# Kernel tuning notes

Hardware: AMD Instinct MI355X
Metric: run time of the kernel (lower is better)

Reference implementation:

```python
import jax, jax.numpy as jnp
import numpy as np

N_NODES = 50000
N_EDGES = 800000
LATDIM = 128
HEAD = 4


def setup_inputs() -> dict:
    key = jax.random.key(0)
    k1, k2, k3, k4, k5, k6 = jax.random.split(key, 6)
    scale = 1.0 / np.sqrt(LATDIM)  # xavier-ish scale for the square projections
    return {
        "embeds": jax.random.normal(k1, (N_NODES, LATDIM), dtype=jnp.float32),
        "qW": jax.random.normal(k2, (LATDIM, LATDIM), dtype=jnp.float32) * scale,
        "kW": jax.random.normal(k3, (LATDIM, LATDIM), dtype=jnp.float32) * scale,
        "vW": jax.random.normal(k4, (LATDIM, LATDIM), dtype=jnp.float32) * scale,
        "rows": jax.random.randint(k5, (N_EDGES,), 0, N_NODES, dtype=jnp.int32),
        "cols": jax.random.randint(k6, (N_EDGES,), 0, N_NODES, dtype=jnp.int32),
    }


def reference(embeds, qW, kW, vW, rows, cols):
    n_nodes, latdim = embeds.shape
    head_dim = latdim // HEAD
    rowEmb = embeds[rows]                         # [E, D] gather by dst
    colEmb = embeds[cols]                         # [E, D] gather by src
    q = (rowEmb @ qW).reshape(-1, HEAD, head_dim)  # [E, H, Dh]
    k = (colEmb @ kW).reshape(-1, HEAD, head_dim)
    v = (colEmb @ vW).reshape(-1, HEAD, head_dim)
    att = jnp.einsum('ehd,ehd->eh', q, k)
    att = jnp.clip(att, -10.0, 10.0)
    expAtt = jnp.exp(att)                          # [E, H]
    # segment softmax denominator via scatter-add over destination nodes
    attNorm = jax.ops.segment_sum(expAtt, rows, num_segments=n_nodes)[rows]
    att = expAtt / (attNorm + 1e-8)
    res = (att[:, :, None] * v).reshape(-1, latdim)  # [E, D]
    out = jax.ops.segment_sum(res, rows, num_segments=n_nodes)  # [N, D]
    return out
```

## Files before the change

kernel.cpp:

```cpp
#include <hip/hip_runtime.h>
#include <hip/hip_bf16.h>

#define N_NODES 50000
#define N_EDGES 800000
#define LATDIM 128
#define HEAD 4
#define SLOT_CAP 96

typedef __attribute__((ext_vector_type(8))) short short8;
typedef __attribute__((ext_vector_type(4))) float floatx4;

__device__ __forceinline__ unsigned bf16_rne_bits(float x) {
    unsigned u = __builtin_bit_cast(unsigned, x);
    return (u + 0x7fffu + ((u >> 16) & 1u)) & 0xffff0000u;
}
__device__ __forceinline__ void split_bf16(float x, short& hi, short& lo) {
    unsigned hb = bf16_rne_bits(x);
    hi = (short)(hb >> 16);
    float hf = __builtin_bit_cast(float, hb);
    unsigned lb = bf16_rne_bits(x - hf);
    lo = (short)(lb >> 16);
}

#define SCAT_T ((N_EDGES / 4 + 767) / 768)
#define GEMM_BLOCKS ((N_NODES + 63) / 64)
#define LDSP 136

__global__ __launch_bounds__(768) void gemm_scatter_kernel(
    const float* __restrict__ E,
    const float* __restrict__ qW, const float* __restrict__ kW,
    const float* __restrict__ vW,
    const int* __restrict__ rows, const int* __restrict__ cols,
    int* __restrict__ cnt, int* __restrict__ slots,
    float* __restrict__ Q, unsigned short* __restrict__ KV2)
{
    __shared__ short AhL[64 * LDSP];
    __shared__ short AlL[64 * LDSP];

    if (blockIdx.x < SCAT_T) {
        const int t = blockIdx.x * 768 + threadIdx.x;
        if (t < N_EDGES / 4) {
            int4 r = ((const int4*)rows)[t];
            int4 c = ((const int4*)cols)[t];
            int p;
            p = atomicAdd(&cnt[r.x], 1);
            if (p < SLOT_CAP) slots[(size_t)r.x * SLOT_CAP + p] = c.x;
            p = atomicAdd(&cnt[r.y], 1);
            if (p < SLOT_CAP) slots[(size_t)r.y * SLOT_CAP + p] = c.y;
            p = atomicAdd(&cnt[r.z], 1);
            if (p < SLOT_CAP) slots[(size_t)r.z * SLOT_CAP + p] = c.z;
            p = atomicAdd(&cnt[r.w], 1);
            if (p < SLOT_CAP) slots[(size_t)r.w * SLOT_CAP + p] = c.w;
        }
        return;
    }

    const int r_base = (blockIdx.x - SCAT_T) * 64;

    for (int chnk = threadIdx.x; chnk < 2048; chnk += 768) {
        const int row = chnk >> 5, c4 = chnk & 31;
        int grow = r_base + row;
        if (grow > N_NODES - 1) grow = N_NODES - 1;
        float4 x = ((const float4*)E)[(size_t)grow * 32 + c4];
        short h0, l0, h1, l1, h2, l2, h3, l3;
        split_bf16(x.x, h0, l0);
        split_bf16(x.y, h1, l1);
        split_bf16(x.z, h2, l2);
        split_bf16(x.w, h3, l3);
        *(short4*)(AhL + row * LDSP + c4 * 4) = make_short4(h0, h1, h2, h3);
        *(short4*)(AlL + row * LDSP + c4 * 4) = make_short4(l0, l1, l2, l3);
    }

    const int wave = threadIdx.x >> 6;
    const int lane = threadIdx.x & 63;
    const int which = wave >> 2;
    const int n_base = (wave & 3) * 32;
    const int ln = lane & 15;
    const int q  = lane >> 4;

    const float* W = (which == 0) ? qW : (which == 1) ? kW : vW;
    short8 Bh[2][4], Bl[2][4];
#pragma unroll
    for (int tIdx = 0; tIdx < 2; ++tIdx)
#pragma unroll
        for (int c = 0; c < 4; ++c)
#pragma unroll
            for (int j = 0; j < 8; ++j) {
                float w = W[(c * 32 + q * 8 + j) * 128 + n_base + tIdx * 16 + ln];
                short hi, lo;
                split_bf16(w, hi, lo);
                Bh[tIdx][c][j] = hi;
                Bl[tIdx][c][j] = lo;
            }

    __syncthreads();

    const int vs = (which == 2) ? 32 : 0;
    const int c0 = n_base + ln;
    const int c1 = n_base + 16 + ln;

    for (int rt = 0; rt < 4; ++rt) {
        const short* ah = AhL + (rt * 16 + ln) * LDSP + q * 8;
        const short* al = AlL + (rt * 16 + ln) * LDSP + q * 8;

        floatx4 acc0 = {0.f, 0.f, 0.f, 0.f};
        floatx4 acc1 = {0.f, 0.f, 0.f, 0.f};
#pragma unroll
        for (int c = 0; c < 4; ++c) {
            short8 Ah = *(const short8*)(ah + c * 32);
            short8 Al = *(const short8*)(al + c * 32);
            acc0 = __builtin_amdgcn_mfma_f32_16x16x32_bf16(Ah, Bh[0][c], acc0, 0, 0, 0);
            acc0 = __builtin_amdgcn_mfma_f32_16x16x32_bf16(Ah, Bl[0][c], acc0, 0, 0, 0);
            acc0 = __builtin_amdgcn_mfma_f32_16x16x32_bf16(Al, Bh[0][c], acc0, 0, 0, 0);
            acc1 = __builtin_amdgcn_mfma_f32_16x16x32_bf16(Ah, Bh[1][c], acc1, 0, 0, 0);
            acc1 = __builtin_amdgcn_mfma_f32_16x16x32_bf16(Ah, Bl[1][c], acc1, 0, 0, 0);
            acc1 = __builtin_amdgcn_mfma_f32_16x16x32_bf16(Al, Bh[1][c], acc1, 0, 0, 0);
        }

        const int r0 = r_base + rt * 16;
#pragma unroll
        for (int r = 0; r < 4; ++r) {
            const int row = r0 + q * 4 + r;
            if (row >= N_NODES) continue;
            if (which == 0) {
                Q[(size_t)row * 128 + c0] = acc0[r];
                Q[(size_t)row * 128 + c1] = acc1[r];
            } else {
                KV2[(size_t)row * 256 + (c0 >> 5) * 64 + (c0 & 31) + vs] =
                    (unsigned short)(bf16_rne_bits(acc0[r]) >> 16);
                KV2[(size_t)row * 256 + (c1 >> 5) * 64 + (c1 & 31) + vs] =
                    (unsigned short)(bf16_rne_bits(acc1[r]) >> 16);
            }
        }
    }
}

__global__ __launch_bounds__(256) void fused_kernel(
    const float* __restrict__ Q,
    const unsigned short* __restrict__ KV2,
    const int* __restrict__ cnt,
    const int* __restrict__ slots,
    float* __restrict__ out)
{
    const int n = blockIdx.x * 4 + (threadIdx.x >> 6);
    if (n >= N_NODES) return;
    const int lane = threadIdx.x & 63;
    const int s  = lane & 1;
    const int h  = (lane >> 1) & 3;
    const int el = lane >> 3;

    int deg = cnt[n];
    if (deg > SLOT_CAP) deg = SLOT_CAP;

    float qv[16];
    {
        const float4* qp = (const float4*)(Q + (size_t)n * 128 + h * 32 + s * 16);
#pragma unroll
        for (int j = 0; j < 4; ++j) {
            float4 t = qp[j];
            qv[4 * j + 0] = t.x; qv[4 * j + 1] = t.y;
            qv[4 * j + 2] = t.z; qv[4 * j + 3] = t.w;
        }
    }

    float acc[16];
#pragma unroll
    for (int j = 0; j < 16; ++j) acc[j] = 0.f;
    float norm = 0.f;

    const int* srow = slots + (size_t)n * SLOT_CAP;

    for (int i = 0; i < deg; i += 8) {
        const int e = i + el;
        if (e < deg) {
            const int col = srow[e];
            const unsigned short* kp = KV2 + (size_t)col * 256 + h * 64 + s * 16;
            uint4 k0 = *(const uint4*)(kp);
            uint4 k1 = *(const uint4*)(kp + 8);
            uint4 v0 = *(const uint4*)(kp + 32);
            uint4 v1 = *(const uint4*)(kp + 40);

            unsigned kw[8] = {k0.x, k0.y, k0.z, k0.w, k1.x, k1.y, k1.z, k1.w};
            float p = 0.f;
#pragma unroll
            for (int d = 0; d < 8; ++d) {
                float flo = __builtin_bit_cast(float, kw[d] << 16);
                float fhi = __builtin_bit_cast(float, kw[d] & 0xffff0000u);
                p += qv[2 * d] * flo + qv[2 * d + 1] * fhi;
            }
            p += __shfl_xor(p, 1);

            float a = expf(fminf(fmaxf(p, -10.0f), 10.0f));
            norm += a;

            unsigned vw[8] = {v0.x, v0.y, v0.z, v0.w, v1.x, v1.y, v1.z, v1.w};
#pragma unroll
            for (int d = 0; d < 8; ++d) {
                float flo = __builtin_bit_cast(float, vw[d] << 16);
                float fhi = __builtin_bit_cast(float, vw[d] & 0xffff0000u);
                acc[2 * d]     += a * flo;
                acc[2 * d + 1] += a * fhi;
            }
        }
    }

#pragma unroll
    for (int m = 8; m <= 32; m <<= 1) {
        norm += __shfl_xor(norm, m, 64);
#pragma unroll
        for (int j = 0; j < 16; ++j) acc[j] += __shfl_xor(acc[j], m, 64);
    }

    if (el == 0) {
        const float inv = 1.0f / (norm + 1e-8f);
        float4* op = (float4*)(out + (size_t)n * 128 + h * 32 + s * 16);
#pragma unroll
        for (int j = 0; j < 4; ++j)
            op[j] = make_float4(acc[4 * j] * inv, acc[4 * j + 1] * inv,
                                acc[4 * j + 2] * inv, acc[4 * j + 3] * inv);
    }
}

extern "C" void kernel_launch(void* const* d_in, const int* in_sizes, int n_in,
                              void* d_out, int out_size, void* d_ws, size_t ws_size,
                              hipStream_t stream) {
    const float* embeds = (const float*)d_in[0];
    const float* qW     = (const float*)d_in[1];
    const float* kW     = (const float*)d_in[2];
    const float* vW     = (const float*)d_in[3];
    const int*   rows   = (const int*)d_in[4];
    const int*   cols   = (const int*)d_in[5];
    float* out = (float*)d_out;

    float* Q = (float*)d_ws;
    unsigned short* KV2 = (unsigned short*)(Q + (size_t)N_NODES * LATDIM);
    int* cnt   = (int*)(KV2 + (size_t)N_NODES * 256);
    int* slots = cnt + N_NODES;

    hipMemsetAsync(cnt, 0, sizeof(int) * N_NODES, stream);

    gemm_scatter_kernel<<<SCAT_T + GEMM_BLOCKS, 768, 0, stream>>>(
        embeds, qW, kW, vW, rows, cols, cnt, slots, Q, KV2);

    fused_kernel<<<(N_NODES + 3) / 4, 256, 0, stream>>>(
        Q, KV2, cnt, slots, out);
}
```

Baseline: 211.9 us.

## Merge scatter, GEMM and attention into one persistent cooperative kernel

```diff
diff --git a/kernel.cpp b/kernel.cpp
--- a/kernel.cpp
+++ b/kernel.cpp
@@ -1,11 +1,21 @@
 #include <hip/hip_runtime.h>
 #include <hip/hip_bf16.h>
+#include <hip/hip_cooperative_groups.h>
+
+namespace cg = cooperative_groups;
 
 #define N_NODES 50000
 #define N_EDGES 800000
 #define LATDIM 128
 #define HEAD 4
 #define SLOT_CAP 96
+
+#define BLOCK_T 768
+#define SCAT_UNITS ((N_EDGES / 4 + BLOCK_T - 1) / BLOCK_T)
+#define GEMM_TILES ((N_NODES + 63) / 64)
+#define FUSE_WAVES 12
+#define FUSE_GROUPS ((N_NODES + FUSE_WAVES - 1) / FUSE_WAVES)
+#define LDSP 136
 
 typedef __attribute__((ext_vector_type(8))) short short8;
 typedef __attribute__((ext_vector_type(4))) float floatx4;
@@ -22,62 +32,55 @@
     lo = (short)(lb >> 16);
 }
 
-#define SCAT_T ((N_EDGES / 4 + 767) / 768)
-#define GEMM_BLOCKS ((N_NODES + 63) / 64)
-#define LDSP 136
-
-__global__ __launch_bounds__(768) void gemm_scatter_kernel(
+__device__ __forceinline__ void scatter_unit(
+    int u, const int* __restrict__ rows, const int* __restrict__ cols,
+    int* __restrict__ cnt, int* __restrict__ slots, int tid)
+{
+    const int t = u * BLOCK_T + tid;
+    if (t < N_EDGES / 4) {
+        int4 r = ((const int4*)rows)[t];
+        int4 c = ((const int4*)cols)[t];
+        int p;
+        p = atomicAdd(&cnt[r.x], 1);
+        if (p < SLOT_CAP) slots[(size_t)r.x * SLOT_CAP + p] = c.x;
+        p = atomicAdd(&cnt[r.y], 1);
+        if (p < SLOT_CAP) slots[(size_t)r.y * SLOT_CAP + p] = c.y;
+        p = atomicAdd(&cnt[r.z], 1);
+        if (p < SLOT_CAP) slots[(size_t)r.z * SLOT_CAP + p] = c.z;
+        p = atomicAdd(&cnt[r.w], 1);
+        if (p < SLOT_CAP) slots[(size_t)r.w * SLOT_CAP + p] = c.w;
+    }
+}
+
+__global__ __launch_bounds__(BLOCK_T) void persist_kernel(
     const float* __restrict__ E,
     const float* __restrict__ qW, const float* __restrict__ kW,
     const float* __restrict__ vW,
     const int* __restrict__ rows, const int* __restrict__ cols,
-    int* __restrict__ cnt, int* __restrict__ slots,
-    float* __restrict__ Q, unsigned short* __restrict__ KV2)
+    int* __restrict__ cnt, int* __restrict__ slots, int* __restrict__ tk,
+    float* __restrict__ Q, unsigned short* __restrict__ KV2,
+    float* __restrict__ out)
 {
     __shared__ short AhL[64 * LDSP];
     __shared__ short AlL[64 * LDSP];
-
-    if (blockIdx.x < SCAT_T) {
-        const int t = blockIdx.x * 768 + threadIdx.x;
-        if (t < N_EDGES / 4) {
-            int4 r = ((const int4*)rows)[t];
-            int4 c = ((const int4*)cols)[t];
-            int p;
-            p = atomicAdd(&cnt[r.x], 1);
-            if (p < SLOT_CAP) slots[(size_t)r.x * SLOT_CAP + p] = c.x;
-            p = atomicAdd(&cnt[r.y], 1);
-            if (p < SLOT_CAP) slots[(size_t)r.y * SLOT_CAP + p] = c.y;
-            p = atomicAdd(&cnt[r.z], 1);
-            if (p < SLOT_CAP) slots[(size_t)r.z * SLOT_CAP + p] = c.z;
-            p = atomicAdd(&cnt[r.w], 1);
-            if (p < SLOT_CAP) slots[(size_t)r.w * SLOT_CAP + p] = c.w;
-        }
-        return;
-    }
-
-    const int r_base = (blockIdx.x - SCAT_T) * 64;
-
-    for (int chnk = threadIdx.x; chnk < 2048; chnk += 768) {
-        const int row = chnk >> 5, c4 = chnk & 31;
-        int grow = r_base + row;
-        if (grow > N_NODES - 1) grow = N_NODES - 1;
-        float4 x = ((const float4*)E)[(size_t)grow * 32 + c4];
-        short h0, l0, h1, l1, h2, l2, h3, l3;
-        split_bf16(x.x, h0, l0);
-        split_bf16(x.y, h1, l1);
-        split_bf16(x.z, h2, l2);
-        split_bf16(x.w, h3, l3);
-        *(short4*)(AhL + row * LDSP + c4 * 4) = make_short4(h0, h1, h2, h3);
-        *(short4*)(AlL + row * LDSP + c4 * 4) = make_short4(l0, l1, l2, l3);
-    }
-
-    const int wave = threadIdx.x >> 6;
-    const int lane = threadIdx.x & 63;
-    const int which = wave >> 2;
+    __shared__ int s_g;
+
+    const int tid  = threadIdx.x;
+    const int wave = tid >> 6;
+    const int lane = tid & 63;
+
+    if (tid == 0) s_g = atomicAdd(&tk[0], 1);
+    __syncthreads();
+    {
+        const int su = s_g;
+        __syncthreads();
+        if (su < SCAT_UNITS) scatter_unit(su, rows, cols, cnt, slots, tid);
+    }
+
+    const int which  = wave >> 2;
     const int n_base = (wave & 3) * 32;
     const int ln = lane & 15;
     const int q  = lane >> 4;
-
     const float* W = (which == 0) ? qW : (which == 1) ? kW : vW;
     short8 Bh[2][4], Bl[2][4];
 #pragma unroll
@@ -93,131 +96,164 @@
                 Bl[tIdx][c][j] = lo;
             }
 
-    __syncthreads();
-
     const int vs = (which == 2) ? 32 : 0;
     const int c0 = n_base + ln;
     const int c1 = n_base + 16 + ln;
 
-    for (int rt = 0; rt < 4; ++rt) {
-        const short* ah = AhL + (rt * 16 + ln) * LDSP + q * 8;
-        const short* al = AlL + (rt * 16 + ln) * LDSP + q * 8;
-
-        floatx4 acc0 = {0.f, 0.f, 0.f, 0.f};
-        floatx4 acc1 = {0.f, 0.f, 0.f, 0.f};
-#pragma unroll
-        for (int c = 0; c < 4; ++c) {
-            short8 Ah = *(const short8*)(ah + c * 32);
-            short8 Al = *(const short8*)(al + c * 32);
-            acc0 = __builtin_amdgcn_mfma_f32_16x16x32_bf16(Ah, Bh[0][c], acc0, 0, 0, 0);
-            acc0 = __builtin_amdgcn_mfma_f32_16x16x32_bf16(Ah, Bl[0][c], acc0, 0, 0, 0);
-            acc0 = __builtin_amdgcn_mfma_f32_16x16x32_bf16(Al, Bh[0][c], acc0, 0, 0, 0);
-            acc1 = __builtin_amdgcn_mfma_f32_16x16x32_bf16(Ah, Bh[1][c], acc1, 0, 0, 0);
-            acc1 = __builtin_amdgcn_mfma_f32_16x16x32_bf16(Ah, Bl[1][c], acc1, 0, 0, 0);
-            acc1 = __builtin_amdgcn_mfma_f32_16x16x32_bf16(Al, Bh[1][c], acc1, 0, 0, 0);
+    for (;;) {
+        if (tid == 0) s_g = atomicAdd(&tk[1], 1);
+        __syncthreads();
+        const int tile = s_g;
+        __syncthreads();
+        if (tile >= GEMM_TILES) break;
+
+        const int r_base = tile * 64;
+        for (int chnk = tid; chnk < 2048; chnk += BLOCK_T) {
+            const int row = chnk >> 5, c4 = chnk & 31;
+            int grow = r_base + row;
+            if (grow > N_NODES - 1) grow = N_NODES - 1;
+            float4 x = ((const float4*)E)[(size_t)grow * 32 + c4];
+            short h0, l0, h1, l1, h2, l2, h3, l3;
+            split_bf16(x.x, h0, l0);
+            split_bf16(x.y, h1, l1);
+            split_bf16(x.z, h2, l2);
+            split_bf16(x.w, h3, l3);
+            *(short4*)(AhL + row * LDSP + c4 * 4) = make_short4(h0, h1, h2, h3);
+            *(short4*)(AlL + row * LDSP + c4 * 4) = make_short4(l0, l1, l2, l3);
         }
-
-        const int r0 = r_base + rt * 16;
-#pragma unroll
-        for (int r = 0; r < 4; ++r) {
-            const int row = r0 + q * 4 + r;
-            if (row >= N_NODES) continue;
-            if (which == 0) {
-                Q[(size_t)row * 128 + c0] = acc0[r];
-                Q[(size_t)row * 128 + c1] = acc1[r];
-            } else {
-                KV2[(size_t)row * 256 + (c0 >> 5) * 64 + (c0 & 31) + vs] =
-                    (unsigned short)(bf16_rne_bits(acc0[r]) >> 16);
-                KV2[(size_t)row * 256 + (c1 >> 5) * 64 + (c1 & 31) + vs] =
-                    (unsigned short)(bf16_rne_bits(acc1[r]) >> 16);
+        __syncthreads();
+
+        for (int rt = 0; rt < 4; ++rt) {
+            const short* ah = AhL + (rt * 16 + ln) * LDSP + q * 8;
+            const short* al = AlL + (rt * 16 + ln) * LDSP + q * 8;
+
+            floatx4 acc0 = {0.f, 0.f, 0.f, 0.f};
+            floatx4 acc1 = {0.f, 0.f, 0.f, 0.f};
+#pragma unroll
+            for (int c = 0; c < 4; ++c) {
+                short8 Ah = *(const short8*)(ah + c * 32);
+                short8 Al = *(const short8*)(al + c * 32);
+                acc0 = __builtin_amdgcn_mfma_f32_16x16x32_bf16(Ah, Bh[0][c], acc0, 0, 0, 0);
+                acc0 = __builtin_amdgcn_mfma_f32_16x16x32_bf16(Ah, Bl[0][c], acc0, 0, 0, 0);
+                acc0 = __builtin_amdgcn_mfma_f32_16x16x32_bf16(Al, Bh[0][c], acc0, 0, 0, 0);
+                acc1 = __builtin_amdgcn_mfma_f32_16x16x32_bf16(Ah, Bh[1][c], acc1, 0, 0, 0);
+                acc1 = __builtin_amdgcn_mfma_f32_16x16x32_bf16(Ah, Bl[1][c], acc1, 0, 0, 0);
+                acc1 = __builtin_amdgcn_mfma_f32_16x16x32_bf16(Al, Bh[1][c], acc1, 0, 0, 0);
+            }
+
+            const int r0 = r_base + rt * 16;
+#pragma unroll
+            for (int r = 0; r < 4; ++r) {
+                const int row = r0 + q * 4 + r;
+                if (row >= N_NODES) continue;
+                if (which == 0) {
+                    Q[(size_t)row * 128 + c0] = acc0[r];
+                    Q[(size_t)row * 128 + c1] = acc1[r];
+                } else {
+                    KV2[(size_t)row * 256 + (c0 >> 5) * 64 + (c0 & 31) + vs] =
+                        (unsigned short)(bf16_rne_bits(acc0[r]) >> 16);
+                    KV2[(size_t)row * 256 + (c1 >> 5) * 64 + (c1 & 31) + vs] =
+                        (unsigned short)(bf16_rne_bits(acc1[r]) >> 16);
+                }
             }
         }
     }
-}
-
-__global__ __launch_bounds__(256) void fused_kernel(
-    const float* __restrict__ Q,
-    const unsigned short* __restrict__ KV2,
-    const int* __restrict__ cnt,
-    const int* __restrict__ slots,
-    float* __restrict__ out)
-{
-    const int n = blockIdx.x * 4 + (threadIdx.x >> 6);
-    if (n >= N_NODES) return;
-    const int lane = threadIdx.x & 63;
+
+    for (;;) {
+        if (tid == 0) s_g = atomicAdd(&tk[0], 1);
+        __syncthreads();
+        const int u = s_g;
+        __syncthreads();
+        if (u >= SCAT_UNITS) break;
+        scatter_unit(u, rows, cols, cnt, slots, tid);
+    }
+
+    __threadfence();
+    cg::this_grid().sync();
+
     const int s  = lane & 1;
     const int h  = (lane >> 1) & 3;
     const int el = lane >> 3;
 
-    int deg = cnt[n];
-    if (deg > SLOT_CAP) deg = SLOT_CAP;
-
-    float qv[16];
-    {
-        const float4* qp = (const float4*)(Q + (size_t)n * 128 + h * 32 + s * 16);
-#pragma unroll
-        for (int j = 0; j < 4; ++j) {
-            float4 t = qp[j];
-            qv[4 * j + 0] = t.x; qv[4 * j + 1] = t.y;
-            qv[4 * j + 2] = t.z; qv[4 * j + 3] = t.w;
+    for (;;) {
+        if (tid == 0) s_g = atomicAdd(&tk[2], 1);
+        __syncthreads();
+        const int g = s_g;
+        __syncthreads();
+        if (g >= FUSE_GROUPS) break;
+        const int n = g * FUSE_WAVES + wave;
+        if (n < N_NODES) {
+            int deg = cnt[n];
+            if (deg > SLOT_CAP) deg = SLOT_CAP;
+
+            float qv[16];
+            {
+                const float4* qp = (const float4*)(Q + (size_t)n * 128 + h * 32 + s * 16);
+#pragma unroll
+                for (int j = 0; j < 4; ++j) {
+                    float4 t = qp[j];
+                    qv[4 * j + 0] = t.x; qv[4 * j + 1] = t.y;
+                    qv[4 * j + 2] = t.z; qv[4 * j + 3] = t.w;
+                }
+            }
+
+            float acc[16];
+#pragma unroll
+            for (int j = 0; j < 16; ++j) acc[j] = 0.f;
+            float norm = 0.f;
+
+            const int* srow = slots + (size_t)n * SLOT_CAP;
+
+            for (int i = 0; i < deg; i += 8) {
+                const int e = i + el;
+                if (e < deg) {
+                    const int col = srow[e];
+                    const unsigned short* kp = KV2 + (size_t)col * 256 + h * 64 + s * 16;
+                    uint4 k0 = *(const uint4*)(kp);
+                    uint4 k1 = *(const uint4*)(kp + 8);
+                    uint4 v0 = *(const uint4*)(kp + 32);
+                    uint4 v1 = *(const uint4*)(kp + 40);
+
+                    unsigned kw[8] = {k0.x, k0.y, k0.z, k0.w, k1.x, k1.y, k1.z, k1.w};
+                    float p = 0.f;
+#pragma unroll
+                    for (int d = 0; d < 8; ++d) {
+                        float flo = __builtin_bit_cast(float, kw[d] << 16);
+                        float fhi = __builtin_bit_cast(float, kw[d] & 0xffff0000u);
+                        p += qv[2 * d] * flo + qv[2 * d + 1] * fhi;
+                    }
+                    p += __shfl_xor(p, 1);
+
+                    float a = expf(fminf(fmaxf(p, -10.0f), 10.0f));
+                    norm += a;
+
+                    unsigned vw[8] = {v0.x, v0.y, v0.z, v0.w, v1.x, v1.y, v1.z, v1.w};
+#pragma unroll
+                    for (int d = 0; d < 8; ++d) {
+                        float flo = __builtin_bit_cast(float, vw[d] << 16);
+                        float fhi = __builtin_bit_cast(float, vw[d] & 0xffff0000u);
+                        acc[2 * d]     += a * flo;
+                        acc[2 * d + 1] += a * fhi;
+                    }
+                }
+            }
+
+#pragma unroll
+            for (int m = 8; m <= 32; m <<= 1) {
+                norm += __shfl_xor(norm, m, 64);
+#pragma unroll
+                for (int j = 0; j < 16; ++j) acc[j] += __shfl_xor(acc[j], m, 64);
+            }
+
+            if (el == 0) {
+                const float inv = 1.0f / (norm + 1e-8f);
+                float4* op = (float4*)(out + (size_t)n * 128 + h * 32 + s * 16);
+#pragma unroll
+                for (int j = 0; j < 4; ++j)
+                    op[j] = make_float4(acc[4 * j] * inv, acc[4 * j + 1] * inv,
+                                        acc[4 * j + 2] * inv, acc[4 * j + 3] * inv);
+            }
         }
-    }
-
-    float acc[16];
-#pragma unroll
-    for (int j = 0; j < 16; ++j) acc[j] = 0.f;
-    float norm = 0.f;
-
-    const int* srow = slots + (size_t)n * SLOT_CAP;
-
-    for (int i = 0; i < deg; i += 8) {
-        const int e = i + el;
-        if (e < deg) {
-            const int col = srow[e];
-            const unsigned short* kp = KV2 + (size_t)col * 256 + h * 64 + s * 16;
-            uint4 k0 = *(const uint4*)(kp);
-            uint4 k1 = *(const uint4*)(kp + 8);
-            uint4 v0 = *(const uint4*)(kp + 32);
-            uint4 v1 = *(const uint4*)(kp + 40);
-
-            unsigned kw[8] = {k0.x, k0.y, k0.z, k0.w, k1.x, k1.y, k1.z, k1.w};
-            float p = 0.f;
-#pragma unroll
-            for (int d = 0; d < 8; ++d) {
-                float flo = __builtin_bit_cast(float, kw[d] << 16);
-                float fhi = __builtin_bit_cast(float, kw[d] & 0xffff0000u);
-                p += qv[2 * d] * flo + qv[2 * d + 1] * fhi;
-            }
-            p += __shfl_xor(p, 1);
-
-            float a = expf(fminf(fmaxf(p, -10.0f), 10.0f));
-            norm += a;
-
-            unsigned vw[8] = {v0.x, v0.y, v0.z, v0.w, v1.x, v1.y, v1.z, v1.w};
-#pragma unroll
-            for (int d = 0; d < 8; ++d) {
-                float flo = __builtin_bit_cast(float, vw[d] << 16);
-                float fhi = __builtin_bit_cast(float, vw[d] & 0xffff0000u);
-                acc[2 * d]     += a * flo;
-                acc[2 * d + 1] += a * fhi;
-            }
-        }
-    }
-
-#pragma unroll
-    for (int m = 8; m <= 32; m <<= 1) {
-        norm += __shfl_xor(norm, m, 64);
-#pragma unroll
-        for (int j = 0; j < 16; ++j) acc[j] += __shfl_xor(acc[j], m, 64);
-    }
-
-    if (el == 0) {
-        const float inv = 1.0f / (norm + 1e-8f);
-        float4* op = (float4*)(out + (size_t)n * 128 + h * 32 + s * 16);
-#pragma unroll
-        for (int j = 0; j < 4; ++j)
-            op[j] = make_float4(acc[4 * j] * inv, acc[4 * j + 1] * inv,
-                                acc[4 * j + 2] * inv, acc[4 * j + 3] * inv);
     }
 }
 
@@ -236,12 +272,24 @@
     unsigned short* KV2 = (unsigned short*)(Q + (size_t)N_NODES * LATDIM);
     int* cnt   = (int*)(KV2 + (size_t)N_NODES * 256);
     int* slots = cnt + N_NODES;
+    int* tk    = slots + (size_t)N_NODES * SLOT_CAP;
 
     hipMemsetAsync(cnt, 0, sizeof(int) * N_NODES, stream);
-
-    gemm_scatter_kernel<<<SCAT_T + GEMM_BLOCKS, 768, 0, stream>>>(
-        embeds, qW, kW, vW, rows, cols, cnt, slots, Q, KV2);
-
-    fused_kernel<<<(N_NODES + 3) / 4, 256, 0, stream>>>(
-        Q, KV2, cnt, slots, out);
-}
+    hipMemsetAsync(tk, 0, sizeof(int) * 8, stream);
+
+    static int nblk = 0;
+    if (nblk == 0) {
+        int per_cu = 0;
+        hipError_t e = hipOccupancyMaxActiveBlocksPerMultiprocessor(
+            &per_cu, reinterpret_cast<const void*>(persist_kernel), BLOCK_T, 0);
+        if (e != hipSuccess || per_cu < 1) per_cu = 1;
+        nblk = per_cu * 256;
+        if (nblk > 2048) nblk = 2048;
+    }
+
+    void* args[] = { (void*)&embeds, (void*)&qW, (void*)&kW, (void*)&vW,
+                     (void*)&rows, (void*)&cols, (void*)&cnt, (void*)&slots,
+                     (void*)&tk, (void*)&Q, (void*)&KV2, (void*)&out };
+    hipLaunchCooperativeKernel(reinterpret_cast<const void*>(persist_kernel),
+                               dim3(nblk), dim3(BLOCK_T), args, 0u, stream);
+}
```

After: 358.9 us. 1.69x slower.

## Split GEMM blocks per projection with 32-row tiles and 256 threads

Applied to the files above, without the earlier changes.

```diff
diff --git a/kernel.cpp b/kernel.cpp
--- a/kernel.cpp
+++ b/kernel.cpp
@@ -22,11 +22,12 @@
     lo = (short)(lb >> 16);
 }
 
-#define SCAT_T ((N_EDGES / 4 + 767) / 768)
-#define GEMM_BLOCKS ((N_NODES + 63) / 64)
+#define SCAT_UNITS ((N_EDGES / 4 + 255) / 256)
+#define TILES_PER_PROJ ((N_NODES + 31) / 32)
+#define GEMM_BLOCKS (3 * TILES_PER_PROJ)
 #define LDSP 136
 
-__global__ __launch_bounds__(768) void gemm_scatter_kernel(
+__global__ __launch_bounds__(256) void gemm_scatter_kernel(
     const float* __restrict__ E,
     const float* __restrict__ qW, const float* __restrict__ kW,
     const float* __restrict__ vW,
@@ -34,11 +35,11 @@
     int* __restrict__ cnt, int* __restrict__ slots,
     float* __restrict__ Q, unsigned short* __restrict__ KV2)
 {
-    __shared__ short AhL[64 * LDSP];
-    __shared__ short AlL[64 * LDSP];
-
-    if (blockIdx.x < SCAT_T) {
-        const int t = blockIdx.x * 768 + threadIdx.x;
+    __shared__ short AhL[32 * LDSP];
+    __shared__ short AlL[32 * LDSP];
+
+    if (blockIdx.x < SCAT_UNITS) {
+        const int t = blockIdx.x * 256 + threadIdx.x;
         if (t < N_EDGES / 4) {
             int4 r = ((const int4*)rows)[t];
             int4 c = ((const int4*)cols)[t];
@@ -55,9 +56,13 @@
         return;
     }
 
-    const int r_base = (blockIdx.x - SCAT_T) * 64;
-
-    for (int chnk = threadIdx.x; chnk < 2048; chnk += 768) {
+    const int b = blockIdx.x - SCAT_UNITS;
+    const int which = b % 3;
+    const int tile  = b / 3;
+    const int r_base = tile * 32;
+
+#pragma unroll 4
+    for (int chnk = threadIdx.x; chnk < 1024; chnk += 256) {
         const int row = chnk >> 5, c4 = chnk & 31;
         int grow = r_base + row;
         if (grow > N_NODES - 1) grow = N_NODES - 1;
@@ -70,18 +75,19 @@
         *(short4*)(AhL + row * LDSP + c4 * 4) = make_short4(h0, h1, h2, h3);
         *(short4*)(AlL + row * LDSP + c4 * 4) = make_short4(l0, l1, l2, l3);
     }
+    __syncthreads();
 
     const int wave = threadIdx.x >> 6;
     const int lane = threadIdx.x & 63;
-    const int which = wave >> 2;
-    const int n_base = (wave & 3) * 32;
+    const int n_base = wave * 32;
     const int ln = lane & 15;
     const int q  = lane >> 4;
-
     const float* W = (which == 0) ? qW : (which == 1) ? kW : vW;
-    short8 Bh[2][4], Bl[2][4];
-#pragma unroll
-    for (int tIdx = 0; tIdx < 2; ++tIdx)
+    const int vs = (which == 2) ? 32 : 0;
+
+#pragma unroll
+    for (int tIdx = 0; tIdx < 2; ++tIdx) {
+        short8 Bh[4], Bl[4];
 #pragma unroll
         for (int c = 0; c < 4; ++c)
 #pragma unroll
@@ -89,47 +95,38 @@
                 float w = W[(c * 32 + q * 8 + j) * 128 + n_base + tIdx * 16 + ln];
                 short hi, lo;
                 split_bf16(w, hi, lo);
-                Bh[tIdx][c][j] = hi;
-                Bl[tIdx][c][j] = lo;
-            }
-
-    __syncthreads();
-
-    const int vs = (which == 2) ? 32 : 0;
-    const int c0 = n_base + ln;
-    const int c1 = n_base + 16 + ln;
-
-    for (int rt = 0; rt < 4; ++rt) {
-        const short* ah = AhL + (rt * 16 + ln) * LDSP + q * 8;
-        const short* al = AlL + (rt * 16 + ln) * LDSP + q * 8;
-
-        floatx4 acc0 = {0.f, 0.f, 0.f, 0.f};
-        floatx4 acc1 = {0.f, 0.f, 0.f, 0.f};
-#pragma unroll
-        for (int c = 0; c < 4; ++c) {
-            short8 Ah = *(const short8*)(ah + c * 32);
-            short8 Al = *(const short8*)(al + c * 32);
-            acc0 = __builtin_amdgcn_mfma_f32_16x16x32_bf16(Ah, Bh[0][c], acc0, 0, 0, 0);
-            acc0 = __builtin_amdgcn_mfma_f32_16x16x32_bf16(Ah, Bl[0][c], acc0, 0, 0, 0);
-            acc0 = __builtin_amdgcn_mfma_f32_16x16x32_bf16(Al, Bh[0][c], acc0, 0, 0, 0);
-            acc1 = __builtin_amdgcn_mfma_f32_16x16x32_bf16(Ah, Bh[1][c], acc1, 0, 0, 0);
-            acc1 = __builtin_amdgcn_mfma_f32_16x16x32_bf16(Ah, Bl[1][c], acc1, 0, 0, 0);
-            acc1 = __builtin_amdgcn_mfma_f32_16x16x32_bf16(Al, Bh[1][c], acc1, 0, 0, 0);
-        }
-
-        const int r0 = r_base + rt * 16;
-#pragma unroll
-        for (int r = 0; r < 4; ++r) {
-            const int row = r0 + q * 4 + r;
-            if (row >= N_NODES) continue;
-            if (which == 0) {
-                Q[(size_t)row * 128 + c0] = acc0[r];
-                Q[(size_t)row * 128 + c1] = acc1[r];
-            } else {
-                KV2[(size_t)row * 256 + (c0 >> 5) * 64 + (c0 & 31) + vs] =
-                    (unsigned short)(bf16_rne_bits(acc0[r]) >> 16);
-                KV2[(size_t)row * 256 + (c1 >> 5) * 64 + (c1 & 31) + vs] =
-                    (unsigned short)(bf16_rne_bits(acc1[r]) >> 16);
+                Bh[c][j] = hi;
+                Bl[c][j] = lo;
+            }
+
+        const int cc = n_base + tIdx * 16 + ln;
+
+#pragma unroll
+        for (int rt = 0; rt < 2; ++rt) {
+            const short* ah = AhL + (rt * 16 + ln) * LDSP + q * 8;
+            const short* al = AlL + (rt * 16 + ln) * LDSP + q * 8;
+
+            floatx4 acc = {0.f, 0.f, 0.f, 0.f};
+#pragma unroll
+            for (int c = 0; c < 4; ++c) {
+                short8 Ah = *(const short8*)(ah + c * 32);
+                short8 Al = *(const short8*)(al + c * 32);
+                acc = __builtin_amdgcn_mfma_f32_16x16x32_bf16(Ah, Bh[c], acc, 0, 0, 0);
+                acc = __builtin_amdgcn_mfma_f32_16x16x32_bf16(Ah, Bl[c], acc, 0, 0, 0);
+                acc = __builtin_amdgcn_mfma_f32_16x16x32_bf16(Al, Bh[c], acc, 0, 0, 0);
+            }
+
+            const int r0 = r_base + rt * 16;
+#pragma unroll
+            for (int r = 0; r < 4; ++r) {
+                const int row = r0 + q * 4 + r;
+                if (row >= N_NODES) continue;
+                if (which == 0) {
+                    Q[(size_t)row * 128 + cc] = acc[r];
+                } else {
+                    KV2[(size_t)row * 256 + (cc >> 5) * 64 + (cc & 31) + vs] =
+                        (unsigned short)(bf16_rne_bits(acc[r]) >> 16);
+                }
             }
         }
     }
@@ -239,7 +236,7 @@
 
     hipMemsetAsync(cnt, 0, sizeof(int) * N_NODES, stream);
 
-    gemm_scatter_kernel<<<SCAT_T + GEMM_BLOCKS, 768, 0, stream>>>(
+    gemm_scatter_kernel<<<SCAT_UNITS + GEMM_BLOCKS, 256, 0, stream>>>(
         embeds, qW, kW, vW, rows, cols, cnt, slots, Q, KV2);
 
     fused_kernel<<<(N_NODES + 3) / 4, 256, 0, stream>>>(
```

Measured after the change: 236.9 us. 11.8% more time.
